# Optimization experiments

Hardware: AMD Instinct MI355X
Metric: run time of the kernel (lower is better)

## Reference

```python
import jax, jax.numpy as jnp
import numpy as np

N = 8192
D = 512
H = 256
K_TOPK = 21  # k + 1 with k = 20
EPS_NORM = 1e-12
EPS_DEG = 1e-10


def setup_inputs() -> dict:
    key = jax.random.key(0)
    ks = jax.random.split(key, 10)
    s = 0.02  # small init scale so similarities are well-behaved
    return {
        "features": jax.random.normal(ks[0], (N, D), jnp.float32),
        "masked_features": jax.random.normal(ks[1], (N, D), jnp.float32),
        "W1": jax.random.normal(ks[2], (D, D), jnp.float32) * s,
        "b1": jax.random.normal(ks[3], (D,), jnp.float32) * s,
        "W2": jax.random.normal(ks[4], (D, D), jnp.float32) * s,
        "b2": jax.random.normal(ks[5], (D,), jnp.float32) * s,
        "Wg1": jax.random.normal(ks[6], (D, H), jnp.float32) * s,
        "bg1": jax.random.normal(ks[7], (H,), jnp.float32) * s,
        "Wg2": jax.random.normal(ks[8], (H, D), jnp.float32) * s,
        "bg2": jax.random.normal(ks[9], (D,), jnp.float32) * s,
    }


def reference(features, masked_features, W1, b1, W2, b2, Wg1, bg1, Wg2, bg2):
    # ---- graph generator MLP ----
    h = jax.nn.relu(features @ W1 + b1)            # [N, D]
    emb = h @ W2 + b2                              # [N, D]
    norm = jnp.linalg.norm(emb, axis=1, keepdims=True)
    emb = emb / jnp.maximum(norm, EPS_NORM)        # F.normalize(dim=1, p=2)
    sim = emb @ emb.T                              # [N, N] cosine similarity

    # ---- top-k mask (k+1 neighbors), zero diagonal ----
    _, idx = jax.lax.top_k(sim, K_TOPK)            # [N, K]
    rows = jnp.arange(N)[:, None]
    mask = jnp.zeros((N, N), sim.dtype).at[rows, idx].set(1.0)
    mask = mask * (1.0 - jnp.eye(N, dtype=sim.dtype))  # fill_diagonal_(0)
    mask = jax.lax.stop_gradient(mask)
    sim = jax.nn.relu(sim * mask)

    # ---- symmetrize ----
    gen_adj = (sim + sim.T) * 0.5                  # [N, N]

    # ---- degree norm: D^{-1/2} (A + I) D^{-1/2} ----
    A = gen_adj + jnp.eye(N, dtype=gen_adj.dtype)
    inv_sqrt_deg = 1.0 / (jnp.sqrt(A.sum(axis=1)) + EPS_DEG)
    A = inv_sqrt_deg[:, None] * A * inv_sqrt_deg[None, :]

    # ---- two dense GCN hops (dropout inert in eval mode) ----
    h1 = jax.nn.relu(A @ (masked_features @ Wg1 + bg1))  # [N, H]
    h3 = A @ (h1 @ Wg2 + bg2)                            # [N, D]
    return h3, gen_adj
```

## Files before the change

### kernel.cpp

```cpp
#include <hip/hip_runtime.h>
#include <cstdint>
#include <cstddef>

#define NN 8192
#define DD 512
#define HH 256
#define KTOP 21
#define CCAP 192
#define CMIN 48
#define ECAP 224
#define NBIN 1024

typedef __attribute__((ext_vector_type(8))) __bf16 bf16x8;
typedef __attribute__((ext_vector_type(4))) float f32x4;

__device__ __forceinline__ unsigned short f2bf(float x) {
    unsigned u = __float_as_uint(x);
    u += 0x7fffu + ((u >> 16) & 1u);
    return (unsigned short)(u >> 16);
}
__device__ __forceinline__ float bf2f(unsigned short h) {
    return __uint_as_float(((unsigned)h) << 16);
}
__device__ __forceinline__ unsigned ordkey(float x) {
    unsigned b = __float_as_uint(x);
    return b ^ (((int)b >> 31) | 0x80000000u);
}

#define GLD16(gp, lp) __builtin_amdgcn_global_load_lds( \
    (const __attribute__((address_space(1))) unsigned int*)(gp), \
    (__attribute__((address_space(3))) unsigned int*)(lp), 16, 0, 0)

template<bool TRANSB, int ACT>
__global__ __launch_bounds__(256)
void sgemm128(const float* __restrict__ A, const float* __restrict__ B,
              const float* __restrict__ bias, float* __restrict__ C,
              int M, int N, int K) {
    constexpr int BM = 128, BN = 128, BK = 16;
    __shared__ float As[BK][BM + 4];
    __shared__ float Bs[BK][BN + 4];

    const int tiles_n = N / BN;
    const int by = blockIdx.x / tiles_n;
    const int bx = blockIdx.x % tiles_n;
    const int row0 = by * BM, col0 = bx * BN;
    const int tid = threadIdx.x;
    const int tx = tid & 15, ty = tid >> 4;

    float acc[8][8];
#pragma unroll
    for (int m = 0; m < 8; ++m)
#pragma unroll
        for (int n = 0; n < 8; ++n) acc[m][n] = 0.f;

    for (int k0 = 0; k0 < K; k0 += BK) {
#pragma unroll
        for (int l = 0; l < 2; ++l) {
            int f = tid + l * 256;
            int r = f >> 2, c4 = f & 3;
            float4 v = *reinterpret_cast<const float4*>(
                A + (size_t)(row0 + r) * K + k0 + c4 * 4);
            As[c4 * 4 + 0][r] = v.x;
            As[c4 * 4 + 1][r] = v.y;
            As[c4 * 4 + 2][r] = v.z;
            As[c4 * 4 + 3][r] = v.w;
        }
        if (TRANSB) {
#pragma unroll
            for (int l = 0; l < 2; ++l) {
                int f = tid + l * 256;
                int r = f >> 2, c4 = f & 3;
                float4 v = *reinterpret_cast<const float4*>(
                    B + (size_t)(col0 + r) * K + k0 + c4 * 4);
                Bs[c4 * 4 + 0][r] = v.x;
                Bs[c4 * 4 + 1][r] = v.y;
                Bs[c4 * 4 + 2][r] = v.z;
                Bs[c4 * 4 + 3][r] = v.w;
            }
        } else {
#pragma unroll
            for (int l = 0; l < 2; ++l) {
                int f = tid + l * 256;
                int kr = f >> 5, n4 = f & 31;
                *reinterpret_cast<float4*>(&Bs[kr][n4 * 4]) =
                    *reinterpret_cast<const float4*>(
                        B + (size_t)(k0 + kr) * N + col0 + n4 * 4);
            }
        }
        __syncthreads();

#pragma unroll
        for (int kk = 0; kk < BK; ++kk) {
            float a[8], b[8];
            *(float4*)&a[0] = *(const float4*)&As[kk][ty * 8];
            *(float4*)&a[4] = *(const float4*)&As[kk][ty * 8 + 4];
            *(float4*)&b[0] = *(const float4*)&Bs[kk][tx * 8];
            *(float4*)&b[4] = *(const float4*)&Bs[kk][tx * 8 + 4];
#pragma unroll
            for (int m = 0; m < 8; ++m)
#pragma unroll
                for (int n = 0; n < 8; ++n)
                    acc[m][n] = fmaf(a[m], b[n], acc[m][n]);
        }
        __syncthreads();
    }

    const int crow = row0 + ty * 8;
    const int ccol = col0 + tx * 8;
    float bv[8];
#pragma unroll
    for (int n = 0; n < 8; ++n) bv[n] = bias ? bias[ccol + n] : 0.f;
#pragma unroll
    for (int m = 0; m < 8; ++m) {
        float o[8];
#pragma unroll
        for (int n = 0; n < 8; ++n) {
            float t = acc[m][n] + bv[n];
            if (ACT == 1) t = fmaxf(t, 0.f);
            o[n] = t;
        }
        *reinterpret_cast<float4*>(C + (size_t)(crow + m) * N + ccol)     = *(float4*)&o[0];
        *reinterpret_cast<float4*>(C + (size_t)(crow + m) * N + ccol + 4) = *(float4*)&o[4];
    }
}

__global__ __launch_bounds__(256)
void rownorm_emit_kernel(float* __restrict__ emb, unsigned short* __restrict__ ehi) {
    const int row = blockIdx.x, tid = threadIdx.x;
    float* rp = emb + (size_t)row * DD;
    float v0 = rp[tid], v1 = rp[tid + 256];
    float sum = v0 * v0 + v1 * v1;
#pragma unroll
    for (int off = 32; off > 0; off >>= 1) sum += __shfl_down(sum, off, 64);
    __shared__ float ws[4];
    __shared__ float sc_sh;
    if ((tid & 63) == 0) ws[tid >> 6] = sum;
    __syncthreads();
    if (tid == 0) {
        float n = sqrtf(ws[0] + ws[1] + ws[2] + ws[3]);
        sc_sh = 1.0f / fmaxf(n, 1e-12f);
    }
    __syncthreads();
    float sc = sc_sh;
    v0 *= sc; v1 *= sc;
    rp[tid] = v0;
    rp[tid + 256] = v1;
    ehi[(size_t)row * DD + tid]       = f2bf(v0);
    ehi[(size_t)row * DD + tid + 256] = f2bf(v1);
}

__global__ __launch_bounds__(256)
void split_kernel(const float* __restrict__ e, unsigned short* __restrict__ hi,
                  unsigned short* __restrict__ lo) {
    const int i = (blockIdx.x * 256 + threadIdx.x) * 4;
    float4 v = *reinterpret_cast<const float4*>(e + i);
    ushort4 h, l;
    h.x = f2bf(v.x); l.x = f2bf(v.x - bf2f(h.x));
    h.y = f2bf(v.y); l.y = f2bf(v.y - bf2f(h.y));
    h.z = f2bf(v.z); l.z = f2bf(v.z - bf2f(h.z));
    h.w = f2bf(v.w); l.w = f2bf(v.w - bf2f(h.w));
    *reinterpret_cast<ushort4*>(hi + i) = h;
    *reinterpret_cast<ushort4*>(lo + i) = l;
}

__global__ __launch_bounds__(256)
void wtrans_kernel(const float* __restrict__ W, unsigned short* __restrict__ Thi,
                   unsigned short* __restrict__ Tlo, int K, int N) {
    int t = blockIdx.x * 256 + threadIdx.x;
    if (t >= K * N) return;
    int k = t / N, n = t - k * N;
    float x = W[t];
    unsigned short h = f2bf(x);
    Thi[(size_t)n * K + k] = h;
    Tlo[(size_t)n * K + k] = f2bf(x - bf2f(h));
}

__global__ __launch_bounds__(256)
void zero_kernel(float4* __restrict__ adj4) {
    const float4 z = {0.f, 0.f, 0.f, 0.f};
    size_t gid = (size_t)blockIdx.x * 256 + threadIdx.x;
    const size_t stride = (size_t)gridDim.x * 256;
    const size_t total = (size_t)NN * NN / 4;
    for (size_t i = gid; i < total; i += stride) adj4[i] = z;
}

__global__ __launch_bounds__(256)
void simgemm_bf16(const unsigned short* __restrict__ Ehi,
                  unsigned short* __restrict__ Cb) {
    const int bid = blockIdx.x;
    const int swz = (bid & 7) * 512 + (bid >> 3);
    const int by = swz >> 6, bx = swz & 63;

    __shared__ unsigned short Ah[128 * 32];
    __shared__ unsigned short Bh[128 * 32];

    const int tid = threadIdx.x, lane = tid & 63, wid = tid >> 6;
    const int wm = wid >> 1, wn = wid & 1;
    const int fr = lane & 15, fq = lane >> 4;
    const int lrow = lane >> 2;
    const int lcol8 = (lane & 3) * 8;

    const size_t arow0 = (size_t)by * 128;
    const size_t brow0 = (size_t)bx * 128;

    f32x4 acc[4][4];
#pragma unroll
    for (int m = 0; m < 4; ++m)
#pragma unroll
        for (int n = 0; n < 4; ++n) acc[m][n] = (f32x4){0.f, 0.f, 0.f, 0.f};

    for (int k0 = 0; k0 < DD; k0 += 32) {
#pragma unroll
        for (int i = 0; i < 2; ++i) {
            const int chunk = wid + i * 4;
            const int grow = chunk * 16 + lrow;
            GLD16(Ehi + (arow0 + grow) * DD + (k0 + lcol8), Ah + chunk * 512);
            GLD16(Ehi + (brow0 + grow) * DD + (k0 + lcol8), Bh + chunk * 512);
        }
        __syncthreads();

        bf16x8 ah[4], bh[4];
#pragma unroll
        for (int mf = 0; mf < 4; ++mf)
            ah[mf] = *(const bf16x8*)&Ah[(wm * 64 + mf * 16 + fr) * 32 + fq * 8];
#pragma unroll
        for (int nf = 0; nf < 4; ++nf)
            bh[nf] = *(const bf16x8*)&Bh[(wn * 64 + nf * 16 + fr) * 32 + fq * 8];
#pragma unroll
        for (int mf = 0; mf < 4; ++mf)
#pragma unroll
            for (int nf = 0; nf < 4; ++nf)
                acc[mf][nf] = __builtin_amdgcn_mfma_f32_16x16x32_bf16(ah[mf], bh[nf], acc[mf][nf], 0, 0, 0);
        __syncthreads();
    }

#pragma unroll
    for (int mf = 0; mf < 4; ++mf) {
#pragma unroll
        for (int nf = 0; nf < 4; ++nf) {
            const size_t row = arow0 + wm * 64 + mf * 16 + fq * 4;
            const int col = bx * 128 + wn * 64 + nf * 16 + fr;
#pragma unroll
            for (int r2 = 0; r2 < 4; ++r2)
                Cb[(row + r2) * NN + col] = f2bf(acc[mf][nf][r2]);
        }
    }
}

template<int KDIM>
__global__ __launch_bounds__(256)
void mfma_nt_bias(const unsigned short* __restrict__ Ahi,
                  const unsigned short* __restrict__ Alo,
                  const unsigned short* __restrict__ Bhi,
                  const unsigned short* __restrict__ Blo,
                  const float* __restrict__ bias, float* __restrict__ C, int N) {
    const int tiles_n = N / 128;
    const int by = blockIdx.x / tiles_n, bx = blockIdx.x % tiles_n;

    __shared__ unsigned short Ah[128 * 32];
    __shared__ unsigned short Al[128 * 32];
    __shared__ unsigned short Bh[128 * 32];
    __shared__ unsigned short Bl[128 * 32];

    const int tid = threadIdx.x, lane = tid & 63, wid = tid >> 6;
    const int wm = wid >> 1, wn = wid & 1;
    const int fr = lane & 15, fq = lane >> 4;
    const int lrow = lane >> 2;
    const int lcol8 = (lane & 3) * 8;

    const size_t arow0 = (size_t)by * 128;
    const size_t brow0 = (size_t)bx * 128;

    f32x4 acc[4][4];
#pragma unroll
    for (int m = 0; m < 4; ++m)
#pragma unroll
        for (int n = 0; n < 4; ++n) acc[m][n] = (f32x4){0.f, 0.f, 0.f, 0.f};

    for (int k0 = 0; k0 < KDIM; k0 += 32) {
#pragma unroll
        for (int i = 0; i < 2; ++i) {
            const int chunk = wid + i * 4;
            const int grow = chunk * 16 + lrow;
            GLD16(Ahi + (arow0 + grow) * KDIM + (k0 + lcol8), Ah + chunk * 512);
            GLD16(Alo + (arow0 + grow) * KDIM + (k0 + lcol8), Al + chunk * 512);
            GLD16(Bhi + (brow0 + grow) * KDIM + (k0 + lcol8), Bh + chunk * 512);
            GLD16(Blo + (brow0 + grow) * KDIM + (k0 + lcol8), Bl + chunk * 512);
        }
        __syncthreads();

        bf16x8 ah[4], al[4], bh[4], bl[4];
#pragma unroll
        for (int mf = 0; mf < 4; ++mf) {
            const int r = wm * 64 + mf * 16 + fr;
            ah[mf] = *(const bf16x8*)&Ah[r * 32 + fq * 8];
            al[mf] = *(const bf16x8*)&Al[r * 32 + fq * 8];
        }
#pragma unroll
        for (int nf = 0; nf < 4; ++nf) {
            const int r = wn * 64 + nf * 16 + fr;
            bh[nf] = *(const bf16x8*)&Bh[r * 32 + fq * 8];
            bl[nf] = *(const bf16x8*)&Bl[r * 32 + fq * 8];
        }
#pragma unroll
        for (int mf = 0; mf < 4; ++mf)
#pragma unroll
            for (int nf = 0; nf < 4; ++nf) {
                acc[mf][nf] = __builtin_amdgcn_mfma_f32_16x16x32_bf16(ah[mf], bh[nf], acc[mf][nf], 0, 0, 0);
                acc[mf][nf] = __builtin_amdgcn_mfma_f32_16x16x32_bf16(ah[mf], bl[nf], acc[mf][nf], 0, 0, 0);
                acc[mf][nf] = __builtin_amdgcn_mfma_f32_16x16x32_bf16(al[mf], bh[nf], acc[mf][nf], 0, 0, 0);
            }
        __syncthreads();
    }

#pragma unroll
    for (int mf = 0; mf < 4; ++mf) {
#pragma unroll
        for (int nf = 0; nf < 4; ++nf) {
            const size_t row = arow0 + wm * 64 + mf * 16 + fq * 4;
            const int col = bx * 128 + wn * 64 + nf * 16 + fr;
            const float bv = bias[col];
#pragma unroll
            for (int r2 = 0; r2 < 4; ++r2)
                C[(row + r2) * N + col] = acc[mf][nf][r2] + bv;
        }
    }
}

__global__ __launch_bounds__(256)
void topk_refine_kernel(const unsigned short* __restrict__ simb,
                        const float* __restrict__ emb,
                        int* __restrict__ tidx, float* __restrict__ tval,
                        int* __restrict__ ecnt, int* __restrict__ elj,
                        float* __restrict__ elv) {
    const int row = blockIdx.x;
    const int tid = threadIdx.x;
    const int lane = tid & 63, wave = tid >> 6;

    const uint4* rp = reinterpret_cast<const uint4*>(simb + (size_t)row * NN);
    uint4 q[4];
#pragma unroll
    for (int t = 0; t < 4; ++t) q[t] = rp[t * 256 + tid];
    unsigned pk[16];
#pragma unroll
    for (int t = 0; t < 4; ++t) {
        pk[t * 4 + 0] = q[t].x; pk[t * 4 + 1] = q[t].y;
        pk[t * 4 + 2] = q[t].z; pk[t * 4 + 3] = q[t].w;
    }

    __shared__ int hist[NBIN];
    for (int b = tid; b < NBIN; b += 256) hist[b] = 0;
    __syncthreads();

    short bins[32];
#pragma unroll
    for (int u = 0; u < 16; ++u) {
        float flo = __uint_as_float(pk[u] << 16);
        float fhi = __uint_as_float(pk[u] & 0xFFFF0000u);
        int blo = (int)(flo * (float)NBIN); blo = max(0, min(NBIN - 1, blo));
        int bhi = (int)(fhi * (float)NBIN); bhi = max(0, min(NBIN - 1, bhi));
        bins[u * 2]     = (short)blo;
        bins[u * 2 + 1] = (short)bhi;
        atomicAdd(&hist[blo], 1);
        atomicAdd(&hist[bhi], 1);
    }
    __syncthreads();

    __shared__ int s_bstar;
    if (wave == 0) {
        int cum = 0, found = -1;
        for (int c0 = NBIN - 1; c0 >= 0 && found < 0; c0 -= 64) {
            int b = c0 - lane;
            int cnt = (b >= 0) ? hist[b] : 0;
            int sc = cnt;
#pragma unroll
            for (int off = 1; off < 64; off <<= 1) {
                int o = __shfl_up(sc, off, 64);
                if (lane >= off) sc += o;
            }
            int chunk_total = __shfl(sc, 63, 64);
            bool hit = (cum + sc >= CMIN);
            unsigned long long mh = __ballot(hit);
            if (mh) found = c0 - (__ffsll((long long)mh) - 1);
            else cum += chunk_total;
        }
        if (found < 0) found = 0;
        if (lane == 0) s_bstar = found;
    }
    __syncthreads();
    const int bstar = s_bstar;

    __shared__ int s_cand[CCAP];
    int cnt = 0;
#pragma unroll
    for (int i = 0; i < 32; ++i) cnt += (bins[i] >= bstar) ? 1 : 0;
    int sc = cnt;
#pragma unroll
    for (int off = 1; off < 64; off <<= 1) {
        int o = __shfl_up(sc, off, 64);
        if (lane >= off) sc += o;
    }
    __shared__ int wtot[4];
    if (lane == 63) wtot[wave] = sc;
    __syncthreads();
    int base = sc - cnt;
#pragma unroll
    for (int w = 0; w < 4; ++w)
        if (w < wave) base += wtot[w];
    int total = wtot[0] + wtot[1] + wtot[2] + wtot[3];

    int pos = base;
#pragma unroll
    for (int u = 0; u < 16; ++u) {
#pragma unroll
        for (int h = 0; h < 2; ++h) {
            if (bins[u * 2 + h] >= bstar) {
                if (pos < CCAP)
                    s_cand[pos] = ((u >> 2) * 256 + tid) * 8 + (u & 3) * 2 + h;
                pos++;
            }
        }
    }
    __syncthreads();
    const int ncand = min(total, CCAP);

    __shared__ float sval[CCAP];
    __shared__ int   sidx[CCAP];
    const float* ei = emb + (size_t)row * DD;
    float4 a0 = reinterpret_cast<const float4*>(ei)[lane * 2];
    float4 a1 = reinterpret_cast<const float4*>(ei)[lane * 2 + 1];

    for (int base2 = wave * 2; base2 < ncand; base2 += 8) {
#pragma unroll
        for (int qq = 0; qq < 2; ++qq) {
            int c = base2 + qq;
            if (c >= ncand) break;
            const int j = s_cand[c];
            const float* ej = emb + (size_t)j * DD;
            float4 b0 = reinterpret_cast<const float4*>(ej)[lane * 2];
            float4 b1 = reinterpret_cast<const float4*>(ej)[lane * 2 + 1];
            float s = 0.f;
            s = fmaf(a0.x, b0.x, s); s = fmaf(a0.y, b0.y, s);
            s = fmaf(a0.z, b0.z, s); s = fmaf(a0.w, b0.w, s);
            s = fmaf(a1.x, b1.x, s); s = fmaf(a1.y, b1.y, s);
            s = fmaf(a1.z, b1.z, s); s = fmaf(a1.w, b1.w, s);
#pragma unroll
            for (int off = 32; off > 0; off >>= 1) s += __shfl_xor(s, off, 64);
            if (lane == 0) { sval[c] = s; sidx[c] = j; }
        }
    }
    __syncthreads();

    __shared__ float selv[KTOP];
    __shared__ int   seli[KTOP];
    if (wave == 0) {
        float v[3]; int id[3];
#pragma unroll
        for (int k = 0; k < 3; ++k) {
            int s = lane + 64 * k;
            if (s < ncand) { v[k] = sval[s]; id[k] = sidx[s]; }
            else           { v[k] = -INFINITY; id[k] = 0x7fffffff; }
        }
#pragma unroll 1
        for (int sel = 0; sel < KTOP; ++sel) {
            float bv = v[0]; int bi = id[0];
#pragma unroll
            for (int k = 1; k < 3; ++k)
                if (v[k] > bv || (v[k] == bv && id[k] < bi)) { bv = v[k]; bi = id[k]; }
#pragma unroll
            for (int off = 1; off < 64; off <<= 1) {
                float ov = __shfl_xor(bv, off, 64);
                int   oi = __shfl_xor(bi, off, 64);
                if (ov > bv || (ov == bv && oi < bi)) { bv = ov; bi = oi; }
            }
            if (lane == 0) { selv[sel] = bv; seli[sel] = bi; }
#pragma unroll
            for (int k = 0; k < 3; ++k)
                if (id[k] == bi) { v[k] = -INFINITY; id[k] = 0x7fffffff; }
        }
    }
    __syncthreads();

    if (tid < KTOP) {
        float bv = selv[tid];
        int   bi = seli[tid];
        tval[(size_t)row * KTOP + tid] = bv;
        tidx[(size_t)row * KTOP + tid] = bi;
        if (bi != row && bi >= 0 && bi < NN && bv > 0.f) {
            float v = bv * 0.5f;
            int pi = atomicAdd(ecnt + row, 1);
            if (pi < ECAP) { elj[(size_t)row * ECAP + pi] = bi; elv[(size_t)row * ECAP + pi] = v; }
            int pj = atomicAdd(ecnt + bi, 1);
            if (pj < ECAP) { elj[(size_t)bi * ECAP + pj] = row; elv[(size_t)bi * ECAP + pj] = v; }
        }
    }
}

__global__ __launch_bounds__(256)
void scatter_dense(const int* __restrict__ tidx, const float* __restrict__ tval,
                   float* __restrict__ adj) {
    int t = blockIdx.x * 256 + threadIdx.x;
    if (t >= NN * KTOP) return;
    int i = t / KTOP;
    int j = tidx[t];
    if (j == i || j < 0) return;
    float v = tval[t];
    if (v <= 0.f) return;
    v *= 0.5f;
    atomicAdd(adj + (size_t)i * NN + j, v);
    atomicAdd(adj + (size_t)j * NN + i, v);
}

__global__ __launch_bounds__(256)
void sortdeg_kernel(int* __restrict__ ej, float* __restrict__ ev,
                    const int* __restrict__ ecnt, const float* __restrict__ adj,
                    float* __restrict__ sdeg) {
    const int row = blockIdx.x, tid = threadIdx.x;
    const int lane = tid & 63, wave = tid >> 6;
    const int nraw = ecnt[row];
    __shared__ float ws[4];

    if (nraw > ECAP) {
        const float4* rp = reinterpret_cast<const float4*>(adj + (size_t)row * NN);
        float sum = 0.f;
        for (int f = tid; f < NN / 4; f += 256) {
            float4 v = rp[f];
            sum += (v.x + v.y) + (v.z + v.w);
        }
#pragma unroll
        for (int off = 32; off > 0; off >>= 1) sum += __shfl_down(sum, off, 64);
        if (lane == 0) ws[wave] = sum;
        __syncthreads();
        if (tid == 0)
            sdeg[row] = 1.0f / (sqrtf(1.0f + ws[0] + ws[1] + ws[2] + ws[3]) + 1e-10f);
        return;
    }

    const int n = nraw;
    __shared__ int   lj[ECAP];
    __shared__ float lv[ECAP];
    __shared__ unsigned long long skey[ECAP];
    __shared__ int   oj[ECAP];
    __shared__ float ov[ECAP];
    if (tid < n) {
        int  jv = ej[(size_t)row * ECAP + tid];
        float vv = ev[(size_t)row * ECAP + tid];
        lj[tid] = jv; lv[tid] = vv;
        skey[tid] = ((unsigned long long)(unsigned)jv << 32) | (unsigned long long)ordkey(vv);
    }
    __syncthreads();
    if (tid < n) {
        unsigned long long mk = skey[tid];
        int rank = 0;
        for (int u = 0; u < n; ++u) {
            unsigned long long ku = skey[u];
            rank += (ku < mk || (ku == mk && u < tid)) ? 1 : 0;
        }
        oj[rank] = lj[tid];
        ov[rank] = lv[tid];
    }
    __syncthreads();
    if (tid < n) {
        ej[(size_t)row * ECAP + tid] = oj[tid];
        ev[(size_t)row * ECAP + tid] = ov[tid];
    }
    if (tid == 0) {
        float deg = 1.0f;
        for (int e = 0; e < n; ++e) deg += ov[e];
        sdeg[row] = 1.0f / (sqrtf(deg) + 1e-10f);
    }
}

template<int COLS, bool DORELU>
__global__ __launch_bounds__(256)
void spmm_edges(const int* __restrict__ ej, const float* __restrict__ ev,
                const int* __restrict__ ecnt, const float* __restrict__ adj,
                const float* __restrict__ sdeg,
                const float* __restrict__ X, float* __restrict__ Y) {
    constexpr int CPT = COLS / 256;
    const int i = blockIdx.x;
    const int tid = threadIdx.x;
    const int lane = tid & 63, wave = tid >> 6;
    const float si = sdeg[i];
    const int nraw = ecnt[i];

    float acc[CPT];
#pragma unroll
    for (int c = 0; c < CPT; ++c) acc[c] = 0.f;

    if (nraw <= ECAP) {
        __shared__ int   s_j[ECAP];
        __shared__ float s_w[ECAP];
        if (tid < nraw) {
            int j = ej[(size_t)i * ECAP + tid];
            s_j[tid] = j;
            s_w[tid] = ev[(size_t)i * ECAP + tid] * sdeg[j];
        }
        __syncthreads();
#pragma unroll 4
        for (int e = 0; e < nraw; ++e) {
            int j = s_j[e];
            float we = s_w[e];
#pragma unroll
            for (int c = 0; c < CPT; ++c)
                acc[c] += we * X[(size_t)j * COLS + tid + c * 256];
        }
    } else {
        __shared__ int   s_j[256];
        __shared__ float s_w[256];
        __shared__ int   s_cnt[4];
        const float* rowp = adj + (size_t)i * NN;
        for (int j0 = 0; j0 < NN; j0 += 256) {
            float w = rowp[j0 + tid];
            bool nz = (w != 0.f);
            unsigned long long m = __ballot(nz);
            unsigned long long ltmask = (lane == 0) ? 0ull : (~0ull >> (64 - lane));
            int pre = __popcll(m & ltmask);
            if (lane == 0) s_cnt[wave] = __popcll(m);
            __syncthreads();
            int base = 0;
#pragma unroll
            for (int q = 0; q < 4; ++q)
                if (q < wave) base += s_cnt[q];
            int total = s_cnt[0] + s_cnt[1] + s_cnt[2] + s_cnt[3];
            if (nz) {
                int p = base + pre;
                s_j[p] = j0 + tid;
                s_w[p] = w * sdeg[j0 + tid];
            }
            __syncthreads();
            for (int e = 0; e < total; ++e) {
                int j = s_j[e];
                float we = s_w[e];
#pragma unroll
                for (int c = 0; c < CPT; ++c)
                    acc[c] += we * X[(size_t)j * COLS + tid + c * 256];
            }
            __syncthreads();
        }
    }

#pragma unroll
    for (int c = 0; c < CPT; ++c) {
        float val = si * (acc[c] + si * X[(size_t)i * COLS + tid + c * 256]);
        if (DORELU) val = fmaxf(val, 0.f);
        Y[(size_t)i * COLS + tid + c * 256] = val;
    }
}

extern "C" void kernel_launch(void* const* d_in, const int* in_sizes, int n_in,
                              void* d_out, int out_size, void* d_ws, size_t ws_size,
                              hipStream_t stream) {
    const float* features = (const float*)d_in[0];
    const float* masked   = (const float*)d_in[1];
    const float* W1  = (const float*)d_in[2];
    const float* b1  = (const float*)d_in[3];
    const float* W2  = (const float*)d_in[4];
    const float* b2  = (const float*)d_in[5];
    const float* Wg1 = (const float*)d_in[6];
    const float* bg1 = (const float*)d_in[7];
    const float* Wg2 = (const float*)d_in[8];
    const float* bg2 = (const float*)d_in[9];

    float* out_h3  = (float*)d_out;
    float* out_adj = (float*)d_out + (size_t)NN * DD;
    unsigned short* simb = (unsigned short*)out_adj;

    float* Areg = (float*)d_ws;
    float* Breg = Areg + (size_t)NN * DD;
    float* tail = Breg + (size_t)NN * DD;

    float* h    = Areg;
    unsigned short* ehi = (unsigned short*)Areg;
    unsigned short* mhi = (unsigned short*)Areg;
    unsigned short* mlo = mhi + (size_t)NN * DD;
    unsigned short* h1hi = (unsigned short*)Areg;
    unsigned short* h1lo = h1hi + (size_t)NN * HH;

    float* emb = Breg;
    float* x1  = Breg;
    float* h1  = Breg + (size_t)NN * HH;
    float* x2  = Breg;

    float* tval = tail;
    int*   tidx = (int*)(tval + (size_t)NN * KTOP);
    float* sdeg = (float*)(tidx + (size_t)NN * KTOP);
    int*   ecnt = (int*)(sdeg + NN);
    int*   elj  = ecnt + NN;
    float* elv  = (float*)(elj + (size_t)NN * ECAP);
    unsigned short* wt1hi = (unsigned short*)(elv + (size_t)NN * ECAP);
    unsigned short* wt1lo = wt1hi + (size_t)HH * DD;
    unsigned short* wt2hi = wt1lo + (size_t)HH * DD;
    unsigned short* wt2lo = wt2hi + (size_t)DD * HH;

    dim3 blk(256);

    sgemm128<false, 1><<<dim3((NN / 128) * (DD / 128)), blk, 0, stream>>>(
        features, W1, b1, h, NN, DD, DD);
    sgemm128<false, 0><<<dim3((NN / 128) * (DD / 128)), blk, 0, stream>>>(
        h, W2, b2, emb, NN, DD, DD);
    rownorm_emit_kernel<<<dim3(NN), blk, 0, stream>>>(emb, ehi);
    simgemm_bf16<<<dim3(4096), blk, 0, stream>>>(ehi, simb);
    hipMemsetAsync(ecnt, 0, (size_t)NN * sizeof(int), stream);
    topk_refine_kernel<<<dim3(NN), blk, 0, stream>>>(
        simb, emb, tidx, tval, ecnt, elj, elv);
    zero_kernel<<<dim3(2048), blk, 0, stream>>>((float4*)out_adj);
    scatter_dense<<<dim3((NN * KTOP + 255) / 256), blk, 0, stream>>>(
        tidx, tval, out_adj);
    sortdeg_kernel<<<dim3(NN), blk, 0, stream>>>(elj, elv, ecnt, out_adj, sdeg);
    split_kernel<<<dim3(NN * DD / 1024), blk, 0, stream>>>(masked, mhi, mlo);
    wtrans_kernel<<<dim3(DD * HH / 256), blk, 0, stream>>>(Wg1, wt1hi, wt1lo, DD, HH);
    mfma_nt_bias<DD><<<dim3((NN / 128) * (HH / 128)), blk, 0, stream>>>(
        mhi, mlo, wt1hi, wt1lo, bg1, x1, HH);
    spmm_edges<HH, true><<<dim3(NN), blk, 0, stream>>>(
        elj, elv, ecnt, out_adj, sdeg, x1, h1);
    split_kernel<<<dim3(NN * HH / 1024), blk, 0, stream>>>(h1, h1hi, h1lo);
    wtrans_kernel<<<dim3(HH * DD / 256), blk, 0, stream>>>(Wg2, wt2hi, wt2lo, HH, DD);
    mfma_nt_bias<HH><<<dim3((NN / 128) * (DD / 128)), blk, 0, stream>>>(
        h1hi, h1lo, wt2hi, wt2lo, bg2, x2, DD);
    spmm_edges<DD, false><<<dim3(NN), blk, 0, stream>>>(
        elj, elv, ecnt, out_adj, sdeg, x2, out_h3);
}
```

Baseline: 745.2 us.

## Fuse adjacency zeroing and edge writes into sort kernel; stage sim stores via LDS

Replaces the separate dense zero pass, atomic scatter and degree kernel with one per-row kernel. It zeroes the row, sorts that row's edge list, computes the degree and writes the merged edge values directly. Atomic scatter and full-row degree summation now run only for rows whose edge list overflowed. The bf16 similarity GEMM epilogue is staged through shared memory so that global stores are coalesced 16-byte writes. The histogram in top-k also skips bin 0, which cuts atomic contention on the low bin but may change candidate selection if too few values land in higher bins.

New measurement: 734.7 us. Within noise of the previous version (-1.4%).

```diff
diff --git a/kernel.cpp b/kernel.cpp
--- a/kernel.cpp
+++ b/kernel.cpp
@@ -10,6 +10,7 @@
 #define CMIN 48
 #define ECAP 224
 #define NBIN 1024
+#define BFLOOR 1
 
 typedef __attribute__((ext_vector_type(8))) __bf16 bf16x8;
 typedef __attribute__((ext_vector_type(4))) float f32x4;
@@ -176,23 +177,15 @@
 }
 
 __global__ __launch_bounds__(256)
-void zero_kernel(float4* __restrict__ adj4) {
-    const float4 z = {0.f, 0.f, 0.f, 0.f};
-    size_t gid = (size_t)blockIdx.x * 256 + threadIdx.x;
-    const size_t stride = (size_t)gridDim.x * 256;
-    const size_t total = (size_t)NN * NN / 4;
-    for (size_t i = gid; i < total; i += stride) adj4[i] = z;
-}
-
-__global__ __launch_bounds__(256)
 void simgemm_bf16(const unsigned short* __restrict__ Ehi,
                   unsigned short* __restrict__ Cb) {
     const int bid = blockIdx.x;
     const int swz = (bid & 7) * 512 + (bid >> 3);
     const int by = swz >> 6, bx = swz & 63;
 
-    __shared__ unsigned short Ah[128 * 32];
-    __shared__ unsigned short Bh[128 * 32];
+    __shared__ unsigned short SB[8192];
+    unsigned short* Ah = SB;
+    unsigned short* Bh = SB + 4096;
 
     const int tid = threadIdx.x, lane = tid & 63, wid = tid >> 6;
     const int wm = wid >> 1, wn = wid & 1;
@@ -235,15 +228,27 @@
     }
 
 #pragma unroll
-    for (int mf = 0; mf < 4; ++mf) {
-#pragma unroll
-        for (int nf = 0; nf < 4; ++nf) {
-            const size_t row = arow0 + wm * 64 + mf * 16 + fq * 4;
-            const int col = bx * 128 + wn * 64 + nf * 16 + fr;
-#pragma unroll
-            for (int r2 = 0; r2 < 4; ++r2)
-                Cb[(row + r2) * NN + col] = f2bf(acc[mf][nf][r2]);
-        }
+    for (int ph = 0; ph < 2; ++ph) {
+        if (wm == ph) {
+#pragma unroll
+            for (int mf = 0; mf < 4; ++mf)
+#pragma unroll
+                for (int nf = 0; nf < 4; ++nf)
+#pragma unroll
+                    for (int r2 = 0; r2 < 4; ++r2)
+                        SB[(mf * 16 + fq * 4 + r2) * 128 + wn * 64 + nf * 16 + fr] =
+                            f2bf(acc[mf][nf][r2]);
+        }
+        __syncthreads();
+#pragma unroll
+        for (int it = 0; it < 4; ++it) {
+            int flat = it * 256 + tid;
+            int rowL = flat >> 4, cc = flat & 15;
+            *reinterpret_cast<uint4*>(
+                &Cb[(arow0 + ph * 64 + rowL) * NN + (size_t)bx * 128 + cc * 8]) =
+                *reinterpret_cast<const uint4*>(&SB[rowL * 128 + cc * 8]);
+        }
+        __syncthreads();
     }
 }
 
@@ -361,8 +366,8 @@
         int bhi = (int)(fhi * (float)NBIN); bhi = max(0, min(NBIN - 1, bhi));
         bins[u * 2]     = (short)blo;
         bins[u * 2 + 1] = (short)bhi;
-        atomicAdd(&hist[blo], 1);
-        atomicAdd(&hist[bhi], 1);
+        if (blo >= BFLOOR) atomicAdd(&hist[blo], 1);
+        if (bhi >= BFLOOR) atomicAdd(&hist[bhi], 1);
     }
     __syncthreads();
 
@@ -497,44 +502,18 @@
 }
 
 __global__ __launch_bounds__(256)
-void scatter_dense(const int* __restrict__ tidx, const float* __restrict__ tval,
-                   float* __restrict__ adj) {
-    int t = blockIdx.x * 256 + threadIdx.x;
-    if (t >= NN * KTOP) return;
-    int i = t / KTOP;
-    int j = tidx[t];
-    if (j == i || j < 0) return;
-    float v = tval[t];
-    if (v <= 0.f) return;
-    v *= 0.5f;
-    atomicAdd(adj + (size_t)i * NN + j, v);
-    atomicAdd(adj + (size_t)j * NN + i, v);
-}
-
-__global__ __launch_bounds__(256)
-void sortdeg_kernel(int* __restrict__ ej, float* __restrict__ ev,
-                    const int* __restrict__ ecnt, const float* __restrict__ adj,
-                    float* __restrict__ sdeg) {
+void sort_write_kernel(int* __restrict__ ej, float* __restrict__ ev,
+                       const int* __restrict__ ecnt,
+                       float* __restrict__ adj, float* __restrict__ sdeg) {
     const int row = blockIdx.x, tid = threadIdx.x;
-    const int lane = tid & 63, wave = tid >> 6;
     const int nraw = ecnt[row];
-    __shared__ float ws[4];
-
-    if (nraw > ECAP) {
-        const float4* rp = reinterpret_cast<const float4*>(adj + (size_t)row * NN);
-        float sum = 0.f;
-        for (int f = tid; f < NN / 4; f += 256) {
-            float4 v = rp[f];
-            sum += (v.x + v.y) + (v.z + v.w);
-        }
-#pragma unroll
-        for (int off = 32; off > 0; off >>= 1) sum += __shfl_down(sum, off, 64);
-        if (lane == 0) ws[wave] = sum;
-        __syncthreads();
-        if (tid == 0)
-            sdeg[row] = 1.0f / (sqrtf(1.0f + ws[0] + ws[1] + ws[2] + ws[3]) + 1e-10f);
-        return;
-    }
+
+    float4* out4 = reinterpret_cast<float4*>(adj + (size_t)row * NN);
+    const float4 z = {0.f, 0.f, 0.f, 0.f};
+#pragma unroll
+    for (int f = tid; f < NN / 4; f += 256) out4[f] = z;
+
+    if (nraw > ECAP) return;
 
     const int n = nraw;
     __shared__ int   lj[ECAP];
@@ -569,6 +548,51 @@
         for (int e = 0; e < n; ++e) deg += ov[e];
         sdeg[row] = 1.0f / (sqrtf(deg) + 1e-10f);
     }
+    __syncthreads();
+    if (tid < n) {
+        int j = oj[tid];
+        if (tid == 0 || oj[tid - 1] != j) {
+            float s = ov[tid];
+            if (tid + 1 < n && oj[tid + 1] == j) s += ov[tid + 1];
+            adj[(size_t)row * NN + j] = s;
+        }
+    }
+}
+
+__global__ __launch_bounds__(256)
+void ovf_fix_kernel(const int* __restrict__ tidx, const float* __restrict__ tval,
+                    const int* __restrict__ ecnt, float* __restrict__ adj) {
+    int t = blockIdx.x * 256 + threadIdx.x;
+    if (t >= NN * KTOP) return;
+    int i = t / KTOP;
+    int j = tidx[t];
+    if (j == i || j < 0) return;
+    float v = tval[t];
+    if (v <= 0.f) return;
+    v *= 0.5f;
+    if (ecnt[i] > ECAP) atomicAdd(adj + (size_t)i * NN + j, v);
+    if (ecnt[j] > ECAP) atomicAdd(adj + (size_t)j * NN + i, v);
+}
+
+__global__ __launch_bounds__(256)
+void ovf_deg_kernel(const int* __restrict__ ecnt, const float* __restrict__ adj,
+                    float* __restrict__ sdeg) {
+    const int row = blockIdx.x, tid = threadIdx.x;
+    if (ecnt[row] <= ECAP) return;
+    const int lane = tid & 63, wave = tid >> 6;
+    const float4* rp = reinterpret_cast<const float4*>(adj + (size_t)row * NN);
+    float sum = 0.f;
+    for (int f = tid; f < NN / 4; f += 256) {
+        float4 v = rp[f];
+        sum += (v.x + v.y) + (v.z + v.w);
+    }
+#pragma unroll
+    for (int off = 32; off > 0; off >>= 1) sum += __shfl_down(sum, off, 64);
+    __shared__ float ws[4];
+    if (lane == 0) ws[wave] = sum;
+    __syncthreads();
+    if (tid == 0)
+        sdeg[row] = 1.0f / (sqrtf(1.0f + ws[0] + ws[1] + ws[2] + ws[3]) + 1e-10f);
 }
 
 template<int COLS, bool DORELU>
@@ -704,10 +728,10 @@
     hipMemsetAsync(ecnt, 0, (size_t)NN * sizeof(int), stream);
     topk_refine_kernel<<<dim3(NN), blk, 0, stream>>>(
         simb, emb, tidx, tval, ecnt, elj, elv);
-    zero_kernel<<<dim3(2048), blk, 0, stream>>>((float4*)out_adj);
-    scatter_dense<<<dim3((NN * KTOP + 255) / 256), blk, 0, stream>>>(
-        tidx, tval, out_adj);
-    sortdeg_kernel<<<dim3(NN), blk, 0, stream>>>(elj, elv, ecnt, out_adj, sdeg);
+    sort_write_kernel<<<dim3(NN), blk, 0, stream>>>(elj, elv, ecnt, out_adj, sdeg);
+    ovf_fix_kernel<<<dim3((NN * KTOP + 255) / 256), blk, 0, stream>>>(
+        tidx, tval, ecnt, out_adj);
+    ovf_deg_kernel<<<dim3(NN), blk, 0, stream>>>(ecnt, out_adj, sdeg);
     split_kernel<<<dim3(NN * DD / 1024), blk, 0, stream>>>(masked, mhi, mlo);
     wtrans_kernel<<<dim3(DD * HH / 256), blk, 0, stream>>>(Wg1, wt1hi, wt1lo, DD, HH);
     mfma_nt_bias<DD><<<dim3((NN / 128) * (HH / 128)), blk, 0, stream>>>(
```
